# Optimization experiments

Hardware: AMD Instinct MI355X
Metric: run time of the kernel (lower is better)

The kernel has to match this reference:

```python
import jax, jax.numpy as jnp
import numpy as np

HID = (128, 256, 128)  # nmp_qc NNet hidden layer sizes
D_IN = 256
TARGET = 256


def _mlp_params(key, n_in, n_out, prefix):
    sizes = (n_in,) + HID + (n_out,)
    params = {}
    for i in range(len(sizes) - 1):
        key, k1, k2 = jax.random.split(key, 3)
        fan_in = sizes[i]
        bound = 1.0 / np.sqrt(fan_in)
        params[f"{prefix}_W{i}"] = jax.random.uniform(k1, (sizes[i], sizes[i + 1]), jnp.float32, -bound, bound)
        params[f"{prefix}_b{i}"] = jax.random.uniform(k2, (sizes[i + 1],), jnp.float32, -bound, bound)
    return params, key


def _mlp(x, Ws, bs):
    # ReLU on all layers except the last (linear output), matching NNet
    for i in range(len(Ws) - 1):
        x = jax.nn.relu(x @ Ws[i] + bs[i])
    return x @ Ws[-1] + bs[-1]


def setup_inputs() -> dict:
    key = jax.random.key(0)
    k0, k1, key = jax.random.split(key, 3)
    B, N = 512, 256
    inp = {
        "h0": jax.random.normal(k0, (B, N, D_IN), jnp.float32),
        "hT": jax.random.normal(k1, (B, N, D_IN), jnp.float32),
    }
    gp, key = _mlp_params(key, 2 * D_IN, TARGET, "g")  # gate MLP: concat(h0,hT) -> target
    op, key = _mlp_params(key, D_IN, TARGET, "o")      # value MLP: hT -> target
    inp.update(gp)
    inp.update(op)
    return inp


def reference(h0, hT,
              g_W0, g_b0, g_W1, g_b1, g_W2, g_b2, g_W3, g_b3,
              o_W0, o_b0, o_W1, o_b1, o_W2, o_b2, o_W3, o_b3):
    gWs = (g_W0, g_W1, g_W2, g_W3)
    gbs = (g_b0, g_b1, g_b2, g_b3)
    oWs = (o_W0, o_W1, o_W2, o_W3)
    obs = (o_b0, o_b1, o_b2, o_b3)
    # gate: sigmoid(MLP1([h0; hT])) ; value: MLP2(hT)  -- all [B, N, target]
    gate = jax.nn.sigmoid(_mlp(jnp.concatenate([h0, hT], axis=-1), gWs, gbs))
    val = _mlp(hT, oWs, obs)
    # node validity mask: sum of initial features > 0, matching r_mpnn
    mask = (jnp.sum(h0, axis=-1, keepdims=True) > 0).astype(h0.dtype)  # [B, N, 1]
    return jnp.sum(mask * gate * val, axis=1)  # [B, target]
```

## Files before the change

### kernel.cpp

```cpp
#include <hip/hip_runtime.h>
#include <hip/hip_bf16.h>
#include <stdint.h>


typedef __attribute__((ext_vector_type(8))) short short8_t;
typedef __attribute__((ext_vector_type(16))) float f32x16;

#define ROWS 32
#define NWG  4096
#define NTHR 64

#define SA 132
#define SZ 72

#define OFF_X 0
#define OFF_Z 8448
#define OFF_M 13056
#define LDS_TOTAL 13184

__device__ __forceinline__ short f2bf(float f) {
  union { float f; uint32_t u; } v; v.f = f;
  uint32_t r = (v.u + 0x7FFFu + ((v.u >> 16) & 1u)) >> 16;
  return (short)r;
}

template <int KT16, int KSTEPS, int CT>
__device__ __forceinline__ void gemmW(const short* actin, int Sin,
                                      const short* __restrict__ wsB, int ks0, int cb0,
                                      f32x16 (&acc)[CT], int lane) {
  const int n32 = lane & 31, q32 = lane >> 5;
#pragma unroll
  for (int ks = 0; ks < KSTEPS; ++ks) {
    const int kl = ks * 16 + q32 * 8;
    short8_t b[CT];
#pragma unroll
    for (int ct = 0; ct < CT; ++ct)
      b[ct] = *(const short8_t*)(wsB + (((cb0 + ct) * KT16 + ks0 + ks) << 9) + lane * 8);
    const short8_t a = *(const short8_t*)(actin + n32 * Sin + kl);
#pragma unroll
    for (int ct = 0; ct < CT; ++ct)
      acc[ct] = __builtin_amdgcn_mfma_f32_32x32x16_bf16(a, b[ct], acc[ct], 0, 0, 0);
  }
}

template <int KT16, int CT>
__device__ __forceinline__ void gemmRA(const short8_t (&aR)[8],
                                       const short* __restrict__ wsB, int cb0,
                                       f32x16 (&acc)[CT], int lane) {
#pragma unroll
  for (int ks = 0; ks < 8; ++ks) {
    short8_t b[CT];
#pragma unroll
    for (int ct = 0; ct < CT; ++ct)
      b[ct] = *(const short8_t*)(wsB + (((cb0 + ct) * KT16 + ks) << 9) + lane * 8);
#pragma unroll
    for (int ct = 0; ct < CT; ++ct)
      acc[ct] = __builtin_amdgcn_mfma_f32_32x32x16_bf16(aR[ks], b[ct], acc[ct], 0, 0, 0);
  }
}

template <int CT, int ACTF>
__device__ __forceinline__ void epiW(f32x16 (&acc)[CT], short* actout, int Sout,
                                     const float* __restrict__ bias, int c0,
                                     int n32, int q32) {
#pragma unroll
  for (int ct = 0; ct < CT; ++ct) {
    const int c = c0 + ct * 32 + n32;
    const float bv = bias[c];
#pragma unroll
    for (int reg = 0; reg < 16; ++reg) {
      const int r = (reg & 3) + 8 * (reg >> 2) + 4 * q32;
      float v = acc[ct][reg] + bv;
      if (ACTF == 1) v = fmaxf(v, 0.f);
      actout[r * Sout + c] = f2bf(v);
    }
  }
}

template <bool MASKA>
__device__ __forceinline__ void stage_chunk(const float* __restrict__ src, int row0,
                                            int colbase, short* X, float* maskacc,
                                            int mmode, int lane) {
  const int c4 = lane & 31, rh = lane >> 5;
#pragma unroll
  for (int g = 0; g < 2; ++g) {
    float4 v[8];
#pragma unroll
    for (int it = 0; it < 8; ++it)
      v[it] = *(const float4*)(src + (size_t)(row0 + g * 16 + 2 * it + rh) * 256 + colbase + c4 * 4);
#pragma unroll
    for (int it = 0; it < 8; ++it) {
      const int r = g * 16 + 2 * it + rh;
      short4 pk; pk.x = f2bf(v[it].x); pk.y = f2bf(v[it].y); pk.z = f2bf(v[it].z); pk.w = f2bf(v[it].w);
      *(short4*)(X + r * SA + c4 * 4) = pk;
      if (MASKA && mmode) {
        float s = v[it].x + v[it].y + v[it].z + v[it].w;
        s += __shfl_down(s, 16, 32);
        s += __shfl_down(s, 8, 32);
        s += __shfl_down(s, 4, 32);
        s += __shfl_down(s, 2, 32);
        s += __shfl_down(s, 1, 32);
        if (c4 == 0) {
          if (mmode == 1) maskacc[r] = s; else maskacc[r] += s;
        }
      }
    }
  }
}

template <int NCH, bool MASKA>
__device__ __forceinline__ void streamW(const float* __restrict__ src0,
                                        const float* __restrict__ src1, int splitc,
                                        const short* __restrict__ wsB,
                                        const float* __restrict__ bias,
                                        short* X, float* maskacc,
                                        int row0, int lane) {
  constexpr int KT16 = NCH * 8;
  const int n32 = lane & 31, q32 = lane >> 5;
  f32x16 acc[4];
#pragma unroll
  for (int ct = 0; ct < 4; ++ct) acc[ct] = (f32x16)(0.f);
#pragma unroll
  for (int kc = 0; kc < NCH; ++kc) {
    const bool lo = (kc < splitc);
    const float* src = lo ? src0 : src1;
    const int colbase = (lo ? kc : kc - splitc) * 128;
    const int mm = MASKA ? (kc == 0 ? 1 : (lo ? 2 : 0)) : 0;
    stage_chunk<MASKA>(src, row0, colbase, X, maskacc, mm, lane);
    gemmW<KT16, 8, 4>(X, SA, wsB, kc * 8, 0, acc, lane);
  }
  epiW<4, 1>(acc, X, SA, bias, 0, n32, q32);
}

__device__ __forceinline__ void mid_pair(short* A, short* Z,
                                         const short* __restrict__ ws1,
                                         const float* __restrict__ b1,
                                         const short* __restrict__ ws2,
                                         const float* __restrict__ b2,
                                         int lane) {
  const int n32 = lane & 31, q32 = lane >> 5;
  f32x16 acc2[4];
#pragma unroll
  for (int ct = 0; ct < 4; ++ct) acc2[ct] = (f32x16)(0.f);
#pragma unroll
  for (int q = 0; q < 4; ++q) {
    f32x16 acc1[2];
    acc1[0] = (f32x16)(0.f); acc1[1] = (f32x16)(0.f);
    gemmW<8, 8, 2>(A, SA, ws1, 0, q * 2, acc1, lane);
    epiW<2, 1>(acc1, Z, SZ, b1 + q * 64, 0, n32, q32);
    gemmW<16, 4, 4>(Z, SZ, ws2, q * 4, 0, acc2, lane);
  }
  epiW<4, 1>(acc2, A, SA, b2, 0, n32, q32);
}

__device__ __forceinline__ void final_fuse(const short8_t (&aG)[8], const short* Av,
                                           const short* __restrict__ wsg,
                                           const float* __restrict__ bg,
                                           const short* __restrict__ wsv,
                                           const float* __restrict__ bv,
                                           const float* maskacc, float* __restrict__ out,
                                           int bidx, int lane) {
  const int n32 = lane & 31, q32 = lane >> 5;
#pragma unroll
  for (int q = 0; q < 4; ++q) {
    f32x16 ag[2]; ag[0] = (f32x16)(0.f); ag[1] = (f32x16)(0.f);
    gemmRA<8, 2>(aG, wsg, q * 2, ag, lane);
    f32x16 av[2]; av[0] = (f32x16)(0.f); av[1] = (f32x16)(0.f);
    gemmW<8, 8, 2>(Av, SA, wsv, 0, q * 2, av, lane);
#pragma unroll
    for (int ct = 0; ct < 2; ++ct) {
      const int c = q * 64 + ct * 32 + n32;
      const float gb = bg[c], ob = bv[c];
      float s = 0.f;
#pragma unroll
      for (int reg = 0; reg < 16; ++reg) {
        const int r = (reg & 3) + 8 * (reg >> 2) + 4 * q32;
        if (maskacc[r] > 0.f) {
          const float g = 1.f / (1.f + __expf(-(ag[ct][reg] + gb)));
          s += g * (av[ct][reg] + ob);
        }
      }
      s += __shfl_down(s, 32);
      if (lane < 32) atomicAdd(out + bidx * 256 + c, s);
    }
  }
}

__global__ __launch_bounds__(NTHR, 3)
void readout_main(const float* __restrict__ h0, const float* __restrict__ hT,
                  const short* __restrict__ ws,
                  const float* __restrict__ gb0, const float* __restrict__ gb1,
                  const float* __restrict__ gb2, const float* __restrict__ gb3,
                  const float* __restrict__ ob0, const float* __restrict__ ob1,
                  const float* __restrict__ ob2, const float* __restrict__ ob3,
                  float* __restrict__ out) {
  __shared__ __align__(16) char smem[LDS_TOTAL];
  short* X = (short*)(smem + OFF_X);
  short* Z = (short*)(smem + OFF_Z);
  float* maskacc = (float*)(smem + OFF_M);

  const int lane = threadIdx.x;
  const int row0 = blockIdx.x * ROWS;
  const int bidx = row0 >> 8;
  const int n32 = lane & 31, q32 = lane >> 5;

  streamW<4, true>(h0, hT, 2, ws + 0, gb0, X, maskacc, row0, lane);
  mid_pair(X, Z, ws + 65536, gb1, ws + 98304, gb2, lane);
  short8_t aG[8];
#pragma unroll
  for (int ks = 0; ks < 8; ++ks)
    aG[ks] = *(const short8_t*)(X + n32 * SA + ks * 16 + q32 * 8);
  streamW<2, false>(hT, hT, 2, ws + 163840, ob0, X, maskacc, row0, lane);
  mid_pair(X, Z, ws + 196608, ob1, ws + 229376, ob2, lane);
  final_fuse(aG, X, ws + 131072, gb3, ws + 262144, ob3, maskacc, out, bidx, lane);
}

__global__ void prep(const float* __restrict__ W0, const float* __restrict__ W1,
                     const float* __restrict__ W2, const float* __restrict__ W3,
                     const float* __restrict__ W4, const float* __restrict__ W5,
                     const float* __restrict__ W6, const float* __restrict__ W7,
                     short* __restrict__ ws, float* __restrict__ out) {
  const int l = blockIdx.y;
  const int le = blockIdx.x * 256 + threadIdx.x;
  if (l == 1) { out[le] = 0.f; out[le + 65536] = 0.f; }
  int K, N, off; const float* W;
  switch (l) {
    case 0:  K = 512; N = 128; off = 0;      W = W0; break;
    case 1:  K = 128; N = 256; off = 65536;  W = W1; break;
    case 2:  K = 256; N = 128; off = 98304;  W = W2; break;
    case 3:  K = 128; N = 256; off = 131072; W = W3; break;
    case 4:  K = 256; N = 128; off = 163840; W = W4; break;
    case 5:  K = 128; N = 256; off = 196608; W = W5; break;
    case 6:  K = 256; N = 128; off = 229376; W = W6; break;
    default: K = 128; N = 256; off = 262144; W = W7; break;
  }
  if (le >= K * N) return;
  const int j = le & 7;
  const int lanei = (le >> 3) & 63;
  const int blk = le >> 9;
  const int kt16 = K >> 4;
  const int ks = blk % kt16, cb = blk / kt16;
  const int n = cb * 32 + (lanei & 31);
  const int k = ks * 16 + (lanei >> 5) * 8 + j;
  ws[off + le] = f2bf(W[k * N + n]);
}

extern "C" void kernel_launch(void* const* d_in, const int* in_sizes, int n_in,
                              void* d_out, int out_size, void* d_ws, size_t ws_size,
                              hipStream_t stream) {
  const float* h0  = (const float*)d_in[0];
  const float* hT  = (const float*)d_in[1];
  const float* gW0 = (const float*)d_in[2];  const float* gb0 = (const float*)d_in[3];
  const float* gW1 = (const float*)d_in[4];  const float* gb1 = (const float*)d_in[5];
  const float* gW2 = (const float*)d_in[6];  const float* gb2 = (const float*)d_in[7];
  const float* gW3 = (const float*)d_in[8];  const float* gb3 = (const float*)d_in[9];
  const float* oW0 = (const float*)d_in[10]; const float* ob0 = (const float*)d_in[11];
  const float* oW1 = (const float*)d_in[12]; const float* ob1 = (const float*)d_in[13];
  const float* oW2 = (const float*)d_in[14]; const float* ob2 = (const float*)d_in[15];
  const float* oW3 = (const float*)d_in[16]; const float* ob3 = (const float*)d_in[17];
  float* out = (float*)d_out;
  short* ws  = (short*)d_ws;

  prep<<<dim3(256, 8), 256, 0, stream>>>(gW0, gW1, gW2, gW3, oW0, oW1, oW2, oW3, ws, out);
  readout_main<<<NWG, NTHR, 0, stream>>>(h0, hT, ws,
                                         gb0, gb1, gb2, gb3,
                                         ob0, ob1, ob2, ob3, out);
}
```

Measured before the change: 465.3 us.

## Shrink LDS staging, load value-MLP input directly to registers, raise occupancy

The middle-layer pair now processes the hidden layer in 32-column slices instead of 64, which halves the Z staging buffer and the total LDS footprint. The value MLP's first layer reads hT rows from global memory straight into MFMA A-operand registers, converting to bf16 in-register instead of staging through LDS. Launch bounds move from 3 to 4 waves per EU to allow more resident workgroups. In exchange there are more, smaller GEMM passes with extra epilogue round-trips through LDS, and possible register pressure or spills under the tighter bound.

```diff
diff --git a/kernel.cpp b/kernel.cpp
--- a/kernel.cpp
+++ b/kernel.cpp
@@ -11,12 +11,12 @@
 #define NTHR 64
 
 #define SA 132
-#define SZ 72
+#define SZ 36
 
 #define OFF_X 0
 #define OFF_Z 8448
-#define OFF_M 13056
-#define LDS_TOTAL 13184
+#define OFF_M 10752
+#define LDS_TOTAL 10880
 
 __device__ __forceinline__ short f2bf(float f) {
   union { float f; uint32_t u; } v; v.f = f;
@@ -132,23 +132,50 @@
   epiW<4, 1>(acc, X, SA, bias, 0, n32, q32);
 }
 
-__device__ __forceinline__ void mid_pair(short* A, short* Z,
-                                         const short* __restrict__ ws1,
-                                         const float* __restrict__ b1,
-                                         const short* __restrict__ ws2,
-                                         const float* __restrict__ b2,
-                                         int lane) {
+__device__ __forceinline__ void valueL0(const float* __restrict__ hT,
+                                        const short* __restrict__ wsB,
+                                        const float* __restrict__ bias,
+                                        short* X, int row0, int lane) {
+  const int n32 = lane & 31, q32 = lane >> 5;
+  f32x16 acc[4];
+#pragma unroll
+  for (int ct = 0; ct < 4; ++ct) acc[ct] = (f32x16)(0.f);
+  const float* rowp = hT + (size_t)(row0 + n32) * 256 + q32 * 8;
+#pragma unroll
+  for (int ks = 0; ks < 16; ++ks) {
+    const float4 u0 = *(const float4*)(rowp + ks * 16);
+    const float4 u1 = *(const float4*)(rowp + ks * 16 + 4);
+    short8_t a;
+    a[0] = f2bf(u0.x); a[1] = f2bf(u0.y); a[2] = f2bf(u0.z); a[3] = f2bf(u0.w);
+    a[4] = f2bf(u1.x); a[5] = f2bf(u1.y); a[6] = f2bf(u1.z); a[7] = f2bf(u1.w);
+    short8_t b[4];
+#pragma unroll
+    for (int ct = 0; ct < 4; ++ct)
+      b[ct] = *(const short8_t*)(wsB + ((ct * 16 + ks) << 9) + lane * 8);
+#pragma unroll
+    for (int ct = 0; ct < 4; ++ct)
+      acc[ct] = __builtin_amdgcn_mfma_f32_32x32x16_bf16(a, b[ct], acc[ct], 0, 0, 0);
+  }
+  epiW<4, 1>(acc, X, SA, bias, 0, n32, q32);
+}
+
+__device__ __forceinline__ void mid_pair32(short* A, short* Z,
+                                           const short* __restrict__ ws1,
+                                           const float* __restrict__ b1,
+                                           const short* __restrict__ ws2,
+                                           const float* __restrict__ b2,
+                                           int lane) {
   const int n32 = lane & 31, q32 = lane >> 5;
   f32x16 acc2[4];
 #pragma unroll
   for (int ct = 0; ct < 4; ++ct) acc2[ct] = (f32x16)(0.f);
 #pragma unroll
-  for (int q = 0; q < 4; ++q) {
-    f32x16 acc1[2];
-    acc1[0] = (f32x16)(0.f); acc1[1] = (f32x16)(0.f);
-    gemmW<8, 8, 2>(A, SA, ws1, 0, q * 2, acc1, lane);
-    epiW<2, 1>(acc1, Z, SZ, b1 + q * 64, 0, n32, q32);
-    gemmW<16, 4, 4>(Z, SZ, ws2, q * 4, 0, acc2, lane);
+  for (int q = 0; q < 8; ++q) {
+    f32x16 a1[1];
+    a1[0] = (f32x16)(0.f);
+    gemmW<8, 8, 1>(A, SA, ws1, 0, q, a1, lane);
+    epiW<1, 1>(a1, Z, SZ, b1 + q * 32, 0, n32, q32);
+    gemmW<16, 2, 4>(Z, SZ, ws2, q * 2, 0, acc2, lane);
   }
   epiW<4, 1>(acc2, A, SA, b2, 0, n32, q32);
 }
@@ -186,7 +213,7 @@
   }
 }
 
-__global__ __launch_bounds__(NTHR, 3)
+__global__ __launch_bounds__(NTHR, 4)
 void readout_main(const float* __restrict__ h0, const float* __restrict__ hT,
                   const short* __restrict__ ws,
                   const float* __restrict__ gb0, const float* __restrict__ gb1,
@@ -205,13 +232,13 @@
   const int n32 = lane & 31, q32 = lane >> 5;
 
   streamW<4, true>(h0, hT, 2, ws + 0, gb0, X, maskacc, row0, lane);
-  mid_pair(X, Z, ws + 65536, gb1, ws + 98304, gb2, lane);
+  mid_pair32(X, Z, ws + 65536, gb1, ws + 98304, gb2, lane);
   short8_t aG[8];
 #pragma unroll
   for (int ks = 0; ks < 8; ++ks)
     aG[ks] = *(const short8_t*)(X + n32 * SA + ks * 16 + q32 * 8);
-  streamW<2, false>(hT, hT, 2, ws + 163840, ob0, X, maskacc, row0, lane);
-  mid_pair(X, Z, ws + 196608, ob1, ws + 229376, ob2, lane);
+  valueL0(hT, ws + 163840, ob0, X, row0, lane);
+  mid_pair32(X, Z, ws + 196608, ob1, ws + 229376, ob2, lane);
   final_fuse(aG, X, ws + 131072, gb3, ws + 262144, ob3, maskacc, out, bidx, lane);
 }
 
```

Result: slower. 674.3 us (+44.9%).
